# Performance work log

Hardware: AMD Instinct MI355X
Metric: run time of the kernel (lower is better)

The kernel has to match this reference:

```python
import jax, jax.numpy as jnp
import numpy as np

N_ETYPES = 4


def setup_inputs() -> dict:
    key = jax.random.key(0)
    ks = jax.random.split(key, 6)
    N, E, F = 50000, 800000, 128
    x = jax.random.normal(ks[0], (N, F), dtype=jnp.float32)
    edge_index = jax.random.randint(ks[1], (2, E), 0, N, dtype=jnp.int64)
    edge_type = jax.random.randint(ks[2], (E,), 0, N_ETYPES, dtype=jnp.int64)
    scale = 1.0 / np.sqrt(F)
    W_self = jax.random.normal(ks[3], (N_ETYPES, F, F), dtype=jnp.float32) * scale
    W_neigh = jax.random.normal(ks[4], (N_ETYPES, F, F), dtype=jnp.float32) * scale
    b = jnp.zeros((N_ETYPES, F), dtype=jnp.float32)
    return {"x": x, "edge_index": edge_index, "edge_type": edge_type,
            "W_self": W_self, "W_neigh": W_neigh, "b": b}


def reference(x, edge_index, edge_type, W_self, W_neigh, b):
    # HeteroConv: per-edge-type SageConv (mean aggregation), then mean over types.
    N = x.shape[0]
    src, dst = edge_index[0], edge_index[1]
    msg = x[src]                                   # [E, F] gathered source features
    outs = []
    for t in range(N_ETYPES):                      # small fixed loop over edge types
        w = (edge_type == t).astype(x.dtype)[:, None]          # [E, 1] type mask
        agg = jax.ops.segment_sum(msg * w, dst, num_segments=N)  # [N, F]
        cnt = jax.ops.segment_sum(w, dst, num_segments=N)        # [N, 1]
        mean_agg = agg / jnp.maximum(cnt, 1.0)
        outs.append(x @ W_self[t] + mean_agg @ W_neigh[t] + b[t])
    out = jnp.stack(outs, axis=0)                  # [n_etypes, N, F]
    return out.mean(axis=0)                        # reduction='mean' over edge types
```

## Files before the change

kernel.cpp:

```cpp
#include <hip/hip_runtime.h>

#define FDIM 128
#define NT 4
#define KDIM (FDIM * (NT + 1))
#define GBM 64

#define RSH 6
#define RNODES 64
#define RCAP 1280
#define NBKT 256
#define CHUNK 4096

typedef __attribute__((ext_vector_type(8))) _Float16 h8v;
typedef __attribute__((ext_vector_type(4))) float f4v;

__device__ __forceinline__ unsigned short f2h(float f) {
    _Float16 h = (_Float16)f;
    return __builtin_bit_cast(unsigned short, h);
}
__device__ __forceinline__ void gload_lds16(const void* g, void* l) {
    __builtin_amdgcn_global_load_lds(
        (const __attribute__((address_space(1))) unsigned int*)g,
        (__attribute__((address_space(3))) unsigned int*)l, 16, 0, 0);
}

__global__ __launch_bounds__(256) void x2h(const float* __restrict__ x,
                                           unsigned short* __restrict__ xh, int n4) {
    int i = blockIdx.x * blockDim.x + threadIdx.x;
    if (i < n4) {
        float4 v = reinterpret_cast<const float4*>(x)[i];
        ushort4 o;
        o.x = f2h(v.x);
        o.y = f2h(v.y);
        o.z = f2h(v.z);
        o.w = f2h(v.w);
        reinterpret_cast<ushort4*>(xh)[i] = o;
    }
}

__global__ void mix_weights(const float* __restrict__ Wself,
                            const float* __restrict__ Wneigh,
                            const float* __restrict__ b,
                            unsigned short* __restrict__ WmixT,
                            float* __restrict__ bmean) {
    int i = blockIdx.x * blockDim.x + threadIdx.x;
    if (i >= KDIM * FDIM) return;
    int k = i / FDIM, j = i % FDIM;
    float v;
    if (k < FDIM) {
        v = 0.25f * (Wself[(size_t)(0 * FDIM + k) * FDIM + j] +
                     Wself[(size_t)(1 * FDIM + k) * FDIM + j] +
                     Wself[(size_t)(2 * FDIM + k) * FDIM + j] +
                     Wself[(size_t)(3 * FDIM + k) * FDIM + j]);
    } else {
        int t = (k - FDIM) >> 7;
        int kk = (k - FDIM) & (FDIM - 1);
        v = 0.25f * Wneigh[((size_t)t * FDIM + kk) * FDIM + j];
    }
    WmixT[(size_t)j * KDIM + k] = f2h(v);
    if (i < FDIM) {
        bmean[i] = 0.25f * (b[i] + b[FDIM + i] + b[2 * FDIM + i] + b[3 * FDIM + i]);
    }
}

__global__ __launch_bounds__(256) void k_bin(
    const int* __restrict__ ei, const int* __restrict__ et,
    int* __restrict__ cur, unsigned int* __restrict__ bin,
    int N, int E, int NR) {
    __shared__ int lcnt[1024];
    __shared__ int lpos[1024];
    const int tid = threadIdx.x;
    const int e0 = blockIdx.x * CHUNK;

    for (int b = tid; b < NR; b += 256) lcnt[b] = 0;
    __syncthreads();

    int rs[16];
    unsigned int recs[16];
#pragma unroll
    for (int i = 0; i < 16; ++i) {
        int e = e0 + i * 256 + tid;
        if (e < E) {
            int src = ei[e];
            int dst = ei[E + e];
            int t = et[e];
            rs[i] = dst >> RSH;
            recs[i] = (unsigned int)src |
                      ((unsigned int)(dst & (RNODES - 1)) << 16) |
                      ((unsigned int)t << 22);
            atomicAdd(&lcnt[rs[i]], 1);
        } else {
            rs[i] = -1;
            recs[i] = 0;
        }
    }
    __syncthreads();

    for (int b = tid; b < NR; b += 256) {
        int c = lcnt[b];
        lpos[b] = (c > 0) ? atomicAdd(&cur[b * 16], c) : 0;
    }
    __syncthreads();

#pragma unroll
    for (int i = 0; i < 16; ++i) {
        if (rs[i] >= 0) {
            int p = atomicAdd(&lpos[rs[i]], 1);
            if (p < RCAP) bin[(size_t)rs[i] * RCAP + p] = recs[i];
        }
    }
}

__global__ __launch_bounds__(256) void k_fused(
    const unsigned short* __restrict__ xh, const int* __restrict__ cur,
    const unsigned int* __restrict__ bin, const unsigned short* __restrict__ WmixT,
    const float* __restrict__ bmean, float* __restrict__ out, int N) {
    __shared__ unsigned int recs[RCAP];
    __shared__ unsigned short srcs[RCAP];
    __shared__ int cnts[NBKT];
    __shared__ int scanb[NBKT];
    __shared__ int boff[NBKT];
    __shared__ int cur2[NBKT];
    __shared__ unsigned short magg[RNODES * FDIM];
    __shared__ unsigned short As[GBM * 32];
    __shared__ unsigned short Bs[FDIM * 32];

    const int r = blockIdx.x;
    const int tid = threadIdx.x;

    int K = cur[r * 16];
    if (K > RCAP) K = RCAP;
    for (int i = tid; i < K; i += 256) recs[i] = bin[(size_t)r * RCAP + i];
    cnts[tid] = 0;
    __syncthreads();
    for (int i = tid; i < K; i += 256) {
        unsigned int rec = recs[i];
        int b = ((rec >> 22) << 6) | ((rec >> 16) & 63);
        atomicAdd(&cnts[b], 1);
    }
    __syncthreads();
    int v = cnts[tid];
    scanb[tid] = v;
    __syncthreads();
    for (int off = 1; off < NBKT; off <<= 1) {
        int tv = (tid >= off) ? scanb[tid - off] : 0;
        __syncthreads();
        scanb[tid] += tv;
        __syncthreads();
    }
    boff[tid] = scanb[tid] - v;
    cur2[tid] = scanb[tid] - v;
    __syncthreads();
    for (int i = tid; i < K; i += 256) {
        unsigned int rec = recs[i];
        int b = ((rec >> 22) << 6) | ((rec >> 16) & 63);
        int p = atomicAdd(&cur2[b], 1);
        srcs[p] = (unsigned short)(rec & 0xffffu);
    }

    const int wid = tid >> 6, lane = tid & 63;
    const int wr = wid >> 1, wc = wid & 1;
    const int n0 = r * GBM;
    const int r16 = lane & 15, kg = lane >> 4;
    const int g = tid >> 4, ln = tid & 15;

    f4v acc[2][4];
#pragma unroll
    for (int m = 0; m < 2; ++m)
#pragma unroll
        for (int n = 0; n < 4; ++n) acc[m][n] = (f4v){0.f, 0.f, 0.f, 0.f};
    __syncthreads();

#pragma unroll 1
    for (int ks = 0; ks < 4; ++ks) {
        int k0 = ks * 32;
        {
            int row = tid >> 2, c = tid & 3;
            int cs = c ^ ((row >> 1) & 3);
            int rg = n0 + row; if (rg >= N) rg = N - 1;
            gload_lds16(xh + (size_t)rg * FDIM + k0 + cs * 8, &As[wid * 512]);
        }
#pragma unroll
        for (int p = 0; p < 2; ++p) {
            int ck = p * 256 + tid;
            int col = ck >> 2, c = ck & 3;
            int cs = c ^ ((col >> 1) & 3);
            gload_lds16(WmixT + (size_t)col * KDIM + k0 + cs * 8,
                        &Bs[(p * 4 + wid) * 512]);
        }
        __syncthreads();
        h8v af[2], bfr[4];
#pragma unroll
        for (int m = 0; m < 2; ++m) {
            int row = wr * 32 + m * 16 + r16;
            af[m] = *reinterpret_cast<const h8v*>(
                &As[row * 32 + ((kg ^ ((row >> 1) & 3)) << 3)]);
        }
#pragma unroll
        for (int n = 0; n < 4; ++n) {
            int col = wc * 64 + n * 16 + r16;
            bfr[n] = *reinterpret_cast<const h8v*>(
                &Bs[col * 32 + ((kg ^ ((col >> 1) & 3)) << 3)]);
        }
#pragma unroll
        for (int m = 0; m < 2; ++m)
#pragma unroll
            for (int n = 0; n < 4; ++n)
                acc[m][n] = __builtin_amdgcn_mfma_f32_16x16x32_f16(
                    af[m], bfr[n], acc[m][n], 0, 0, 0);
        __syncthreads();
    }

#pragma unroll 1
    for (int t = 0; t < 4; ++t) {
#pragma unroll 1
        for (int it = 0; it < 4; ++it) {
            int dl = it * 16 + g;
            int b = (t << 6) | dl;
            int beg = boff[b], m = cnts[b];
            h8v a = (h8v)(_Float16)0.f;
            h8v bb = (h8v)(_Float16)0.f;
            int i = 0;
            for (; i + 2 <= m; i += 2) {
                int s0 = srcs[beg + i];
                int s1 = srcs[beg + i + 1];
                a  += *reinterpret_cast<const h8v*>(xh + (size_t)s0 * FDIM + ln * 8);
                bb += *reinterpret_cast<const h8v*>(xh + (size_t)s1 * FDIM + ln * 8);
            }
            if (i < m) {
                int s0 = srcs[beg + i];
                a += *reinterpret_cast<const h8v*>(xh + (size_t)s0 * FDIM + ln * 8);
            }
            float rc = (m > 0) ? 1.0f / (float)m : 0.0f;
            h8v o = (a + bb) * (_Float16)rc;
            *reinterpret_cast<h8v*>(&magg[dl * FDIM + ((ln ^ (dl & 15)) << 3)]) = o;
        }
        __syncthreads();

#pragma unroll 1
        for (int ks = 0; ks < 4; ++ks) {
            int k0 = FDIM + t * FDIM + ks * 32;
#pragma unroll
            for (int p = 0; p < 2; ++p) {
                int ck = p * 256 + tid;
                int col = ck >> 2, c = ck & 3;
                int cs = c ^ ((col >> 1) & 3);
                gload_lds16(WmixT + (size_t)col * KDIM + k0 + cs * 8,
                            &Bs[(p * 4 + wid) * 512]);
            }
            __syncthreads();
            h8v af[2], bfr[4];
#pragma unroll
            for (int m = 0; m < 2; ++m) {
                int row = wr * 32 + m * 16 + r16;
                af[m] = *reinterpret_cast<const h8v*>(
                    &magg[row * FDIM + (((ks * 4 + kg) ^ (row & 15)) << 3)]);
            }
#pragma unroll
            for (int n = 0; n < 4; ++n) {
                int col = wc * 64 + n * 16 + r16;
                bfr[n] = *reinterpret_cast<const h8v*>(
                    &Bs[col * 32 + ((kg ^ ((col >> 1) & 3)) << 3)]);
            }
#pragma unroll
            for (int m = 0; m < 2; ++m)
#pragma unroll
                for (int n = 0; n < 4; ++n)
                    acc[m][n] = __builtin_amdgcn_mfma_f32_16x16x32_f16(
                        af[m], bfr[n], acc[m][n], 0, 0, 0);
            __syncthreads();
        }
    }

    float bm[4];
#pragma unroll
    for (int n = 0; n < 4; ++n) bm[n] = bmean[wc * 64 + n * 16 + r16];
#pragma unroll
    for (int m = 0; m < 2; ++m) {
#pragma unroll
        for (int j = 0; j < 4; ++j) {
            int row = n0 + wr * 32 + m * 16 + kg * 4 + j;
            if (row < N) {
                float* o = out + (size_t)row * FDIM;
#pragma unroll
                for (int n = 0; n < 4; ++n)
                    o[wc * 64 + n * 16 + r16] = acc[m][n][j] + bm[n];
            }
        }
    }
}

extern "C" void kernel_launch(void* const* d_in, const int* in_sizes, int n_in,
                              void* d_out, int out_size, void* d_ws, size_t ws_size,
                              hipStream_t stream) {
    const float* x      = (const float*)d_in[0];
    const int*   ei     = (const int*)d_in[1];
    const int*   et     = (const int*)d_in[2];
    const float* Wself  = (const float*)d_in[3];
    const float* Wneigh = (const float*)d_in[4];
    const float* b      = (const float*)d_in[5];
    float* out = (float*)d_out;

    const int N = in_sizes[0] / FDIM;
    const int E = in_sizes[2];
    const int NR = (N + RNODES - 1) >> RSH;

    char* ws = (char*)d_ws;
    unsigned short* xh    = (unsigned short*)ws;
    unsigned short* WmixT = xh + (size_t)N * FDIM;
    float* bmean = (float*)(WmixT + (size_t)FDIM * KDIM);
    int* cur     = (int*)(bmean + FDIM);
    unsigned int* bin = (unsigned int*)(cur + (size_t)NR * 16);

    hipMemsetAsync(cur, 0, (size_t)NR * 16 * sizeof(int), stream);

    x2h<<<(N * FDIM / 4 + 255) / 256, 256, 0, stream>>>(x, xh, N * FDIM / 4);

    mix_weights<<<(KDIM * FDIM + 255) / 256, 256, 0, stream>>>(Wself, Wneigh, b, WmixT, bmean);

    k_bin<<<(E + CHUNK - 1) / CHUNK, 256, 0, stream>>>(ei, et, cur, bin, N, E, NR);

    k_fused<<<NR, 256, 0, stream>>>(xh, cur, bin, WmixT, bmean, out, N);
}
```

Before: 91.03 us.

## Merge prep kernels into one launch and stage full-K tiles in fused kernel

The three preprocessing kernels (fp16 conversion of x, weight mixing, edge binning) become a single launch that dispatches on block index, cutting launch gaps. The fused kernel now loads full 128-wide A and B tiles once per phase instead of 32-wide slices, which removes most per-k-step barriers. It also reuses one aliased shared buffer for records, A tile and aggregated features, replaces the block-wide scan with a warp-shuffle scan, unrolls the gather four ways, and adds a launch-bounds occupancy hint. The larger tiles raise per-block shared memory, and aliasing the A tile as the aggregation buffer needs careful barrier placement.

```diff
diff --git a/kernel.cpp b/kernel.cpp
--- a/kernel.cpp
+++ b/kernel.cpp
@@ -24,114 +24,106 @@
         (__attribute__((address_space(3))) unsigned int*)l, 16, 0, 0);
 }
 
-__global__ __launch_bounds__(256) void x2h(const float* __restrict__ x,
-                                           unsigned short* __restrict__ xh, int n4) {
-    int i = blockIdx.x * blockDim.x + threadIdx.x;
-    if (i < n4) {
-        float4 v = reinterpret_cast<const float4*>(x)[i];
-        ushort4 o;
-        o.x = f2h(v.x);
-        o.y = f2h(v.y);
-        o.z = f2h(v.z);
-        o.w = f2h(v.w);
-        reinterpret_cast<ushort4*>(xh)[i] = o;
-    }
-}
-
-__global__ void mix_weights(const float* __restrict__ Wself,
-                            const float* __restrict__ Wneigh,
-                            const float* __restrict__ b,
-                            unsigned short* __restrict__ WmixT,
-                            float* __restrict__ bmean) {
-    int i = blockIdx.x * blockDim.x + threadIdx.x;
-    if (i >= KDIM * FDIM) return;
-    int k = i / FDIM, j = i % FDIM;
-    float v;
-    if (k < FDIM) {
-        v = 0.25f * (Wself[(size_t)(0 * FDIM + k) * FDIM + j] +
-                     Wself[(size_t)(1 * FDIM + k) * FDIM + j] +
-                     Wself[(size_t)(2 * FDIM + k) * FDIM + j] +
-                     Wself[(size_t)(3 * FDIM + k) * FDIM + j]);
-    } else {
-        int t = (k - FDIM) >> 7;
-        int kk = (k - FDIM) & (FDIM - 1);
-        v = 0.25f * Wneigh[((size_t)t * FDIM + kk) * FDIM + j];
-    }
-    WmixT[(size_t)j * KDIM + k] = f2h(v);
-    if (i < FDIM) {
-        bmean[i] = 0.25f * (b[i] + b[FDIM + i] + b[2 * FDIM + i] + b[3 * FDIM + i]);
-    }
-}
-
-__global__ __launch_bounds__(256) void k_bin(
-    const int* __restrict__ ei, const int* __restrict__ et,
-    int* __restrict__ cur, unsigned int* __restrict__ bin,
-    int N, int E, int NR) {
+__global__ __launch_bounds__(256) void k_prep(
+    const float* __restrict__ x, const int* __restrict__ ei,
+    const int* __restrict__ et, const float* __restrict__ Wself,
+    const float* __restrict__ Wneigh, const float* __restrict__ bvec,
+    unsigned short* __restrict__ xh, unsigned short* __restrict__ WmixT,
+    float* __restrict__ bmean, int* __restrict__ cur,
+    unsigned int* __restrict__ bin, int N, int E, int NR, int nbBin, int nbX) {
     __shared__ int lcnt[1024];
     __shared__ int lpos[1024];
+    const int bid = blockIdx.x;
     const int tid = threadIdx.x;
-    const int e0 = blockIdx.x * CHUNK;
-
-    for (int b = tid; b < NR; b += 256) lcnt[b] = 0;
-    __syncthreads();
-
-    int rs[16];
-    unsigned int recs[16];
-#pragma unroll
-    for (int i = 0; i < 16; ++i) {
-        int e = e0 + i * 256 + tid;
-        if (e < E) {
-            int src = ei[e];
-            int dst = ei[E + e];
-            int t = et[e];
-            rs[i] = dst >> RSH;
-            recs[i] = (unsigned int)src |
-                      ((unsigned int)(dst & (RNODES - 1)) << 16) |
-                      ((unsigned int)t << 22);
-            atomicAdd(&lcnt[rs[i]], 1);
-        } else {
-            rs[i] = -1;
-            recs[i] = 0;
-        }
-    }
-    __syncthreads();
-
-    for (int b = tid; b < NR; b += 256) {
-        int c = lcnt[b];
-        lpos[b] = (c > 0) ? atomicAdd(&cur[b * 16], c) : 0;
-    }
-    __syncthreads();
-
-#pragma unroll
-    for (int i = 0; i < 16; ++i) {
-        if (rs[i] >= 0) {
-            int p = atomicAdd(&lpos[rs[i]], 1);
-            if (p < RCAP) bin[(size_t)rs[i] * RCAP + p] = recs[i];
-        }
-    }
-}
-
-__global__ __launch_bounds__(256) void k_fused(
+
+    if (bid < nbBin) {
+        const int e0 = bid * CHUNK;
+        for (int b = tid; b < NR; b += 256) lcnt[b] = 0;
+        __syncthreads();
+        int rs[16];
+        unsigned int recs[16];
+#pragma unroll
+        for (int i = 0; i < 16; ++i) {
+            int e = e0 + i * 256 + tid;
+            if (e < E) {
+                int src = ei[e];
+                int dst = ei[E + e];
+                int t = et[e];
+                rs[i] = dst >> RSH;
+                recs[i] = (unsigned int)src |
+                          ((unsigned int)(dst & (RNODES - 1)) << 16) |
+                          ((unsigned int)t << 22);
+                atomicAdd(&lcnt[rs[i]], 1);
+            } else { rs[i] = -1; recs[i] = 0; }
+        }
+        __syncthreads();
+        for (int b = tid; b < NR; b += 256) {
+            int c = lcnt[b];
+            lpos[b] = (c > 0) ? atomicAdd(&cur[b * 16], c) : 0;
+        }
+        __syncthreads();
+#pragma unroll
+        for (int i = 0; i < 16; ++i) {
+            if (rs[i] >= 0) {
+                int p = atomicAdd(&lpos[rs[i]], 1);
+                if (p < RCAP) bin[(size_t)rs[i] * RCAP + p] = recs[i];
+            }
+        }
+    } else if (bid < nbBin + nbX) {
+        int i = (bid - nbBin) * 256 + tid;
+        int n8 = N * FDIM / 8;
+        if (i < n8) {
+            float4 v0 = reinterpret_cast<const float4*>(x)[i * 2];
+            float4 v1 = reinterpret_cast<const float4*>(x)[i * 2 + 1];
+            ushort4 o0, o1;
+            o0.x = f2h(v0.x); o0.y = f2h(v0.y); o0.z = f2h(v0.z); o0.w = f2h(v0.w);
+            o1.x = f2h(v1.x); o1.y = f2h(v1.y); o1.z = f2h(v1.z); o1.w = f2h(v1.w);
+            reinterpret_cast<ushort4*>(xh)[i * 2] = o0;
+            reinterpret_cast<ushort4*>(xh)[i * 2 + 1] = o1;
+        }
+    } else {
+        int i = (bid - nbBin - nbX) * 256 + tid;
+        if (i < KDIM * FDIM) {
+            int k = i / FDIM, j = i % FDIM;
+            float v;
+            if (k < FDIM) {
+                v = 0.25f * (Wself[(size_t)(0 * FDIM + k) * FDIM + j] +
+                             Wself[(size_t)(1 * FDIM + k) * FDIM + j] +
+                             Wself[(size_t)(2 * FDIM + k) * FDIM + j] +
+                             Wself[(size_t)(3 * FDIM + k) * FDIM + j]);
+            } else {
+                int t = (k - FDIM) >> 7;
+                int kk = (k - FDIM) & (FDIM - 1);
+                v = 0.25f * Wneigh[((size_t)t * FDIM + kk) * FDIM + j];
+            }
+            WmixT[(size_t)j * KDIM + k] = f2h(v);
+            if (i < FDIM)
+                bmean[i] = 0.25f * (bvec[i] + bvec[FDIM + i] +
+                                    bvec[2 * FDIM + i] + bvec[3 * FDIM + i]);
+        }
+    }
+}
+
+__global__ __launch_bounds__(256, 3) void k_fused(
     const unsigned short* __restrict__ xh, const int* __restrict__ cur,
     const unsigned int* __restrict__ bin, const unsigned short* __restrict__ WmixT,
     const float* __restrict__ bmean, float* __restrict__ out, int N) {
-    __shared__ unsigned int recs[RCAP];
-    __shared__ unsigned short srcs[RCAP];
-    __shared__ int cnts[NBKT];
-    __shared__ int scanb[NBKT];
-    __shared__ int boff[NBKT];
-    __shared__ int cur2[NBKT];
-    __shared__ unsigned short magg[RNODES * FDIM];
-    __shared__ unsigned short As[GBM * 32];
-    __shared__ unsigned short Bs[FDIM * 32];
+    __shared__ __align__(16) char smem[53760];
+    unsigned int* recs    = (unsigned int*)smem;
+    unsigned short* Atile = (unsigned short*)smem;
+    unsigned short* Btile = (unsigned short*)(smem + 16384);
+    unsigned short* srcs  = (unsigned short*)(smem + 49152);
+    int* cnts             = (int*)(smem + 51712);
+    int* offb             = (int*)(smem + 52736);
 
     const int r = blockIdx.x;
     const int tid = threadIdx.x;
+    const int n0 = r * GBM;
 
     int K = cur[r * 16];
     if (K > RCAP) K = RCAP;
     for (int i = tid; i < K; i += 256) recs[i] = bin[(size_t)r * RCAP + i];
-    cnts[tid] = 0;
+    if (tid < NBKT) cnts[tid] = 0;
     __syncthreads();
     for (int i = tid; i < K; i += 256) {
         unsigned int rec = recs[i];
@@ -139,28 +131,32 @@
         atomicAdd(&cnts[b], 1);
     }
     __syncthreads();
-    int v = cnts[tid];
-    scanb[tid] = v;
-    __syncthreads();
-    for (int off = 1; off < NBKT; off <<= 1) {
-        int tv = (tid >= off) ? scanb[tid - off] : 0;
-        __syncthreads();
-        scanb[tid] += tv;
-        __syncthreads();
-    }
-    boff[tid] = scanb[tid] - v;
-    cur2[tid] = scanb[tid] - v;
+    if (tid < 64) {
+        int c0 = cnts[4 * tid], c1 = cnts[4 * tid + 1];
+        int c2 = cnts[4 * tid + 2], c3 = cnts[4 * tid + 3];
+        int tot = c0 + c1 + c2 + c3;
+        int xs = tot;
+        for (int off = 1; off < 64; off <<= 1) {
+            int y = __shfl_up(xs, off, 64);
+            if (tid >= off) xs += y;
+        }
+        int excl = xs - tot;
+        offb[4 * tid] = excl;
+        offb[4 * tid + 1] = excl + c0;
+        offb[4 * tid + 2] = excl + c0 + c1;
+        offb[4 * tid + 3] = excl + c0 + c1 + c2;
+    }
     __syncthreads();
     for (int i = tid; i < K; i += 256) {
         unsigned int rec = recs[i];
         int b = ((rec >> 22) << 6) | ((rec >> 16) & 63);
-        int p = atomicAdd(&cur2[b], 1);
+        int p = atomicAdd(&offb[b], 1);
         srcs[p] = (unsigned short)(rec & 0xffffu);
     }
+    __syncthreads();
 
     const int wid = tid >> 6, lane = tid & 63;
     const int wr = wid >> 1, wc = wid & 1;
-    const int n0 = r * GBM;
     const int r16 = lane & 15, kg = lane >> 4;
     const int g = tid >> 4, ln = tid & 15;
 
@@ -169,106 +165,107 @@
     for (int m = 0; m < 2; ++m)
 #pragma unroll
         for (int n = 0; n < 4; ++n) acc[m][n] = (f4v){0.f, 0.f, 0.f, 0.f};
-    __syncthreads();
-
-#pragma unroll 1
+
+#pragma unroll
+    for (int j = 0; j < 4; ++j) {
+        int fc = j * 256 + tid;
+        int row = fc >> 4, c = fc & 15;
+        int rg = n0 + row; if (rg >= N) rg = N - 1;
+        gload_lds16(xh + (size_t)rg * FDIM + ((c ^ (row & 15)) << 3),
+                    Atile + j * 2048 + wid * 512);
+    }
+#pragma unroll
+    for (int j = 0; j < 8; ++j) {
+        int fc = j * 256 + tid;
+        int col = fc >> 4, c = fc & 15;
+        gload_lds16(WmixT + (size_t)col * KDIM + ((c ^ (col & 15)) << 3),
+                    Btile + j * 2048 + wid * 512);
+    }
+    __syncthreads();
+
+#pragma unroll
     for (int ks = 0; ks < 4; ++ks) {
-        int k0 = ks * 32;
+        int q = ks * 4 + kg;
+        h8v a0, a1, bf[4];
         {
-            int row = tid >> 2, c = tid & 3;
-            int cs = c ^ ((row >> 1) & 3);
-            int rg = n0 + row; if (rg >= N) rg = N - 1;
-            gload_lds16(xh + (size_t)rg * FDIM + k0 + cs * 8, &As[wid * 512]);
-        }
-#pragma unroll
-        for (int p = 0; p < 2; ++p) {
-            int ck = p * 256 + tid;
-            int col = ck >> 2, c = ck & 3;
-            int cs = c ^ ((col >> 1) & 3);
-            gload_lds16(WmixT + (size_t)col * KDIM + k0 + cs * 8,
-                        &Bs[(p * 4 + wid) * 512]);
-        }
-        __syncthreads();
-        h8v af[2], bfr[4];
-#pragma unroll
-        for (int m = 0; m < 2; ++m) {
-            int row = wr * 32 + m * 16 + r16;
-            af[m] = *reinterpret_cast<const h8v*>(
-                &As[row * 32 + ((kg ^ ((row >> 1) & 3)) << 3)]);
+            int row = wr * 32 + r16;
+            a0 = *reinterpret_cast<const h8v*>(&Atile[row * 128 + ((q ^ (row & 15)) << 3)]);
+            row += 16;
+            a1 = *reinterpret_cast<const h8v*>(&Atile[row * 128 + ((q ^ (row & 15)) << 3)]);
         }
 #pragma unroll
         for (int n = 0; n < 4; ++n) {
             int col = wc * 64 + n * 16 + r16;
-            bfr[n] = *reinterpret_cast<const h8v*>(
-                &Bs[col * 32 + ((kg ^ ((col >> 1) & 3)) << 3)]);
-        }
-#pragma unroll
-        for (int m = 0; m < 2; ++m)
-#pragma unroll
-            for (int n = 0; n < 4; ++n)
-                acc[m][n] = __builtin_amdgcn_mfma_f32_16x16x32_f16(
-                    af[m], bfr[n], acc[m][n], 0, 0, 0);
-        __syncthreads();
+            bf[n] = *reinterpret_cast<const h8v*>(&Btile[col * 128 + ((q ^ (col & 15)) << 3)]);
+        }
+#pragma unroll
+        for (int n = 0; n < 4; ++n) {
+            acc[0][n] = __builtin_amdgcn_mfma_f32_16x16x32_f16(a0, bf[n], acc[0][n], 0, 0, 0);
+            acc[1][n] = __builtin_amdgcn_mfma_f32_16x16x32_f16(a1, bf[n], acc[1][n], 0, 0, 0);
+        }
     }
 
 #pragma unroll 1
-    for (int t = 0; t < 4; ++t) {
+    for (int t = 0; t < NT; ++t) {
+        __syncthreads();
+#pragma unroll
+        for (int j = 0; j < 8; ++j) {
+            int fc = j * 256 + tid;
+            int col = fc >> 4, c = fc & 15;
+            gload_lds16(WmixT + (size_t)col * KDIM + (t + 1) * FDIM +
+                            ((c ^ (col & 15)) << 3),
+                        Btile + j * 2048 + wid * 512);
+        }
 #pragma unroll 1
-        for (int it = 0; it < 4; ++it) {
-            int dl = it * 16 + g;
+        for (int u = 0; u < 4; ++u) {
+            int dl = g * 4 + u;
             int b = (t << 6) | dl;
-            int beg = boff[b], m = cnts[b];
-            h8v a = (h8v)(_Float16)0.f;
-            h8v bb = (h8v)(_Float16)0.f;
+            int end = offb[b], m = cnts[b], beg = end - m;
+            h8v a0 = (h8v)(_Float16)0.f, a1 = (h8v)(_Float16)0.f;
+            h8v a2 = (h8v)(_Float16)0.f, a3 = (h8v)(_Float16)0.f;
             int i = 0;
-            for (; i + 2 <= m; i += 2) {
-                int s0 = srcs[beg + i];
-                int s1 = srcs[beg + i + 1];
-                a  += *reinterpret_cast<const h8v*>(xh + (size_t)s0 * FDIM + ln * 8);
-                bb += *reinterpret_cast<const h8v*>(xh + (size_t)s1 * FDIM + ln * 8);
-            }
-            if (i < m) {
-                int s0 = srcs[beg + i];
-                a += *reinterpret_cast<const h8v*>(xh + (size_t)s0 * FDIM + ln * 8);
-            }
+            for (; i + 4 <= m; i += 4) {
+                int s0 = srcs[beg + i],     s1 = srcs[beg + i + 1];
+                int s2 = srcs[beg + i + 2], s3 = srcs[beg + i + 3];
+                a0 += *reinterpret_cast<const h8v*>(xh + (size_t)s0 * FDIM + ln * 8);
+                a1 += *reinterpret_cast<const h8v*>(xh + (size_t)s1 * FDIM + ln * 8);
+                a2 += *reinterpret_cast<const h8v*>(xh + (size_t)s2 * FDIM + ln * 8);
+                a3 += *reinterpret_cast<const h8v*>(xh + (size_t)s3 * FDIM + ln * 8);
+            }
+            if (i + 2 <= m) {
+                int s0 = srcs[beg + i], s1 = srcs[beg + i + 1];
+                a0 += *reinterpret_cast<const h8v*>(xh + (size_t)s0 * FDIM + ln * 8);
+                a1 += *reinterpret_cast<const h8v*>(xh + (size_t)s1 * FDIM + ln * 8);
+                i += 2;
+            }
+            if (i < m)
+                a0 += *reinterpret_cast<const h8v*>(xh + (size_t)srcs[beg + i] * FDIM + ln * 8);
             float rc = (m > 0) ? 1.0f / (float)m : 0.0f;
-            h8v o = (a + bb) * (_Float16)rc;
-            *reinterpret_cast<h8v*>(&magg[dl * FDIM + ((ln ^ (dl & 15)) << 3)]) = o;
-        }
-        __syncthreads();
-
-#pragma unroll 1
+            h8v o = ((a0 + a1) + (a2 + a3)) * (_Float16)rc;
+            *reinterpret_cast<h8v*>(&Atile[dl * 128 + ((ln ^ (dl & 15)) << 3)]) = o;
+        }
+        __syncthreads();
+
+#pragma unroll
         for (int ks = 0; ks < 4; ++ks) {
-            int k0 = FDIM + t * FDIM + ks * 32;
-#pragma unroll
-            for (int p = 0; p < 2; ++p) {
-                int ck = p * 256 + tid;
-                int col = ck >> 2, c = ck & 3;
-                int cs = c ^ ((col >> 1) & 3);
-                gload_lds16(WmixT + (size_t)col * KDIM + k0 + cs * 8,
-                            &Bs[(p * 4 + wid) * 512]);
-            }
-            __syncthreads();
-            h8v af[2], bfr[4];
-#pragma unroll
-            for (int m = 0; m < 2; ++m) {
-                int row = wr * 32 + m * 16 + r16;
-                af[m] = *reinterpret_cast<const h8v*>(
-                    &magg[row * FDIM + (((ks * 4 + kg) ^ (row & 15)) << 3)]);
+            int q = ks * 4 + kg;
+            h8v a0, a1, bf[4];
+            {
+                int row = wr * 32 + r16;
+                a0 = *reinterpret_cast<const h8v*>(&Atile[row * 128 + ((q ^ (row & 15)) << 3)]);
+                row += 16;
+                a1 = *reinterpret_cast<const h8v*>(&Atile[row * 128 + ((q ^ (row & 15)) << 3)]);
             }
 #pragma unroll
             for (int n = 0; n < 4; ++n) {
                 int col = wc * 64 + n * 16 + r16;
-                bfr[n] = *reinterpret_cast<const h8v*>(
-                    &Bs[col * 32 + ((kg ^ ((col >> 1) & 3)) << 3)]);
-            }
-#pragma unroll
-            for (int m = 0; m < 2; ++m)
-#pragma unroll
-                for (int n = 0; n < 4; ++n)
-                    acc[m][n] = __builtin_amdgcn_mfma_f32_16x16x32_f16(
-                        af[m], bfr[n], acc[m][n], 0, 0, 0);
-            __syncthreads();
+                bf[n] = *reinterpret_cast<const h8v*>(&Btile[col * 128 + ((q ^ (col & 15)) << 3)]);
+            }
+#pragma unroll
+            for (int n = 0; n < 4; ++n) {
+                acc[0][n] = __builtin_amdgcn_mfma_f32_16x16x32_f16(a0, bf[n], acc[0][n], 0, 0, 0);
+                acc[1][n] = __builtin_amdgcn_mfma_f32_16x16x32_f16(a1, bf[n], acc[1][n], 0, 0, 0);
+            }
         }
     }
 
@@ -314,11 +311,13 @@
 
     hipMemsetAsync(cur, 0, (size_t)NR * 16 * sizeof(int), stream);
 
-    x2h<<<(N * FDIM / 4 + 255) / 256, 256, 0, stream>>>(x, xh, N * FDIM / 4);
-
-    mix_weights<<<(KDIM * FDIM + 255) / 256, 256, 0, stream>>>(Wself, Wneigh, b, WmixT, bmean);
-
-    k_bin<<<(E + CHUNK - 1) / CHUNK, 256, 0, stream>>>(ei, et, cur, bin, N, E, NR);
+    const int nbBin = (E + CHUNK - 1) / CHUNK;
+    const int nbX   = (N * FDIM / 8 + 255) / 256;
+    const int nbM   = (KDIM * FDIM + 255) / 256;
+
+    k_prep<<<nbBin + nbX + nbM, 256, 0, stream>>>(
+        x, ei, et, Wself, Wneigh, b, xh, WmixT, bmean, cur, bin,
+        N, E, NR, nbBin, nbX);
 
     k_fused<<<NR, 256, 0, stream>>>(xh, cur, bin, WmixT, bmean, out, N);
 }
```

Result: slower. 102.5 us (+12.6%).
